# Optimization experiments

Measured on AMD Instinct MI355X. Metric: run time of the kernel, lower is better.

The kernel has to match this reference:

```python
import jax, jax.numpy as jnp
import numpy as np

B, IN, OUT, E, CTX, DEMO = 32768, 512, 128, 16, 256, 16
HID = IN // 2
GATE_IN = CTX + IN + DEMO  # 784


def setup_inputs() -> dict:
    key = jax.random.key(0)
    ks = jax.random.split(key, 9)
    inp = {
        'x': jax.random.normal(ks[0], (B, IN), dtype=jnp.float32),
        'u': jax.random.normal(ks[1], (B, CTX), dtype=jnp.float32),
        'd': jax.random.normal(ks[2], (B, DEMO), dtype=jnp.float32),
        # gate Linear(GATE_IN -> E)
        'gate_W': jax.random.normal(ks[3], (E, GATE_IN), dtype=jnp.float32) * 0.02,
        'gate_b': jnp.zeros((E,), dtype=jnp.float32),
        # per-expert MLP: Linear(IN->HID), ReLU, Linear(HID->OUT); stacked over experts
        'W1': jax.random.normal(ks[4], (E, HID, IN), dtype=jnp.float32) * 0.02,
        'b1': jnp.zeros((E, HID), dtype=jnp.float32),
        'W2': jax.random.normal(ks[5], (E, OUT, HID), dtype=jnp.float32) * 0.02,
        'b2': jnp.zeros((E, OUT), dtype=jnp.float32),
    }
    return inp


def reference(x, u, d, gate_W, gate_b, W1, b1, W2, b2):
    # gate input = cat([u, x, d], dim=1)  -> [B, GATE_IN]
    g_in = jnp.concatenate([u, x, d], axis=1)
    gate_logits = g_in @ gate_W.T + gate_b            # [B, E]
    weights = jax.nn.softmax(gate_logits, axis=1)     # [B, E]
    # all-expert MLP as batched GEMMs
    h = jax.nn.relu(jnp.einsum('bi,ehi->beh', x, W1) + b1[None])   # [B, E, HID]
    expert_outputs = jnp.einsum('beh,eoh->beo', h, W2) + b2[None]  # [B, E, OUT]
    # mixture_mode == 'logits': weighted sum over experts
    out = jnp.einsum('be,beo->bo', weights, expert_outputs)        # [B, OUT]
    return out
```

## Files before the change

kernel.cpp:

```cpp
#include <hip/hip_runtime.h>

#define B_    32768
#define IN_   512
#define HID_  256
#define OUT_  128
#define E_    16
#define CTX_  256
#define DEMO_ 16
#define GIN_  784

typedef __attribute__((ext_vector_type(8))) short short8;
typedef __attribute__((ext_vector_type(4))) float floatx4;

__device__ __forceinline__ short f2bf(float x){
  unsigned u = __builtin_bit_cast(unsigned, x);
  u += 0x7FFFu + ((u >> 16) & 1u);
  return (short)(u >> 16);
}

__device__ __forceinline__ short8 pack8(float4 a, float4 b){
  short8 r;
  r[0]=f2bf(a.x); r[1]=f2bf(a.y); r[2]=f2bf(a.z); r[3]=f2bf(a.w);
  r[4]=f2bf(b.x); r[5]=f2bf(b.y); r[6]=f2bf(b.z); r[7]=f2bf(b.w);
  return r;
}

__device__ __forceinline__ void load_lds16(const short* g, short* l){
  __builtin_amdgcn_global_load_lds((const __attribute__((address_space(1))) void*)g,
                                   (__attribute__((address_space(3))) void*)l,
                                   16, 0, 0);
}

#define VMCNT8()  asm volatile("s_waitcnt vmcnt(8)"  ::: "memory")
#define VMCNT0()  asm volatile("s_waitcnt vmcnt(0)"  ::: "memory")
#define BAR() do{ asm volatile("" ::: "memory"); __builtin_amdgcn_s_barrier(); \
                  asm volatile("" ::: "memory"); }while(0)
#define LGKM0() do{ asm volatile("s_waitcnt lgkmcnt(0)" ::: "memory"); \
                    __builtin_amdgcn_sched_barrier(0); }while(0)

__device__ __forceinline__ void stage128x64(short* lds, const short* g, int gpitch, int tid){
  const int wvv = tid >> 6, ln = tid & 63;
  const int cb = ln & 7, rsub = ln >> 3;
  #pragma unroll
  for (int i = 0; i < 4; ++i){
    const int r0  = (wvv*4 + i)*8;
    const int row = r0 + rsub;
    const short* gp = g + (size_t)row*gpitch + ((cb ^ rsub) << 3);
    load_lds16(gp, lds + r0*64);
  }
}

__global__ void convert_kernel(const float* __restrict__ x, const float* __restrict__ w1,
                               const float* __restrict__ w2, short* __restrict__ xb,
                               short* __restrict__ w1b, short* __restrict__ w2b){
  const int N1 = B_*IN_, N2 = E_*HID_*IN_, N3 = E_*OUT_*HID_;
  const int total4 = (N1 + N2 + N3) >> 2;
  for (int i = blockIdx.x*blockDim.x + threadIdx.x; i < total4; i += gridDim.x*blockDim.x){
    int e4 = i << 2;
    const float* src; short* dst; int off;
    if (e4 < N1)            { src = x;  dst = xb;  off = e4; }
    else if (e4 < N1 + N2)  { src = w1; dst = w1b; off = e4 - N1; }
    else                    { src = w2; dst = w2b; off = e4 - (N1 + N2); }
    float4 v = *(const float4*)(src + off);
    *(short4*)(dst + off) = make_short4(f2bf(v.x), f2bf(v.y), f2bf(v.z), f2bf(v.w));
  }
}

__global__ __launch_bounds__(256)
void gate_kernel(const float* __restrict__ u, const short* __restrict__ xb,
                 const float* __restrict__ d, const float* __restrict__ gW,
                 const float* __restrict__ gb, float* __restrict__ wout){
  const int tid  = threadIdx.x;
  const int wave = tid >> 6, lane = tid & 63;
  const int l15  = lane & 15, quad = lane >> 4;
  const int row0 = blockIdx.x*64 + wave*16;
  const int rA   = row0 + l15;
  const int kq   = quad*8;

  floatx4 acc  = {0.f,0.f,0.f,0.f};
  floatx4 acc2 = {0.f,0.f,0.f,0.f};

  #pragma unroll
  for (int t = 0; t < 8; ++t){
    const float4 a0 = *(const float4*)&u[(size_t)rA*CTX_ + t*32 + kq];
    const float4 a1 = *(const float4*)&u[(size_t)rA*CTX_ + t*32 + kq + 4];
    const float4 b0 = *(const float4*)&gW[(size_t)l15*GIN_ + t*32 + kq];
    const float4 b1 = *(const float4*)&gW[(size_t)l15*GIN_ + t*32 + kq + 4];
    acc = __builtin_amdgcn_mfma_f32_16x16x32_bf16(pack8(a0,a1), pack8(b0,b1), acc, 0,0,0);
  }
  #pragma unroll
  for (int t = 0; t < 16; ++t){
    const short8 af = *(const short8*)&xb[(size_t)rA*IN_ + t*32 + kq];
    const float4 b0 = *(const float4*)&gW[(size_t)l15*GIN_ + 256 + t*32 + kq];
    const float4 b1 = *(const float4*)&gW[(size_t)l15*GIN_ + 256 + t*32 + kq + 4];
    acc2 = __builtin_amdgcn_mfma_f32_16x16x32_bf16(af, pack8(b0,b1), acc2, 0,0,0);
  }
  {
    short8 af = {0,0,0,0,0,0,0,0}, bf = {0,0,0,0,0,0,0,0};
    if (quad < 2){
      const float4 a0 = *(const float4*)&d[(size_t)rA*DEMO_ + kq];
      const float4 a1 = *(const float4*)&d[(size_t)rA*DEMO_ + kq + 4];
      const float4 b0 = *(const float4*)&gW[(size_t)l15*GIN_ + 768 + kq];
      const float4 b1 = *(const float4*)&gW[(size_t)l15*GIN_ + 768 + kq + 4];
      af = pack8(a0,a1); bf = pack8(b0,b1);
    }
    acc = __builtin_amdgcn_mfma_f32_16x16x32_bf16(af, bf, acc, 0,0,0);
  }

  const float bias = gb[l15];
  #pragma unroll
  for (int r = 0; r < 4; ++r){
    float v = acc[r] + acc2[r] + bias;
    float m = v;
    #pragma unroll
    for (int s = 1; s <= 8; s <<= 1) m = fmaxf(m, __shfl_xor(m, s));
    const float p = __expf(v - m);
    float ssum = p;
    #pragma unroll
    for (int s = 1; s <= 8; s <<= 1) ssum += __shfl_xor(ssum, s);
    wout[(size_t)(row0 + quad*4 + r)*E_ + l15] = p / ssum;
  }
}

__global__ __launch_bounds__(256, 2)
void moe_kernel(const short* __restrict__ xb, const short* __restrict__ w1b,
                const short* __restrict__ w2b, const float* __restrict__ gatew,
                const float* __restrict__ b1g, const float* __restrict__ b2g,
                float* __restrict__ out){
  __shared__ alignas(16) char smem[65536];
  short* s_h  = (short*)smem;
  short* s_w2 = (short*)(smem + 32768);

  const int tid  = threadIdx.x;
  const int wv   = tid >> 6;
  const int lane = tid & 63;
  const int l15  = lane & 15;
  const int hi2  = lane >> 4;
  const int r7   = l15 & 7;
  const int h_off  = (wv >> 1) * 64;
  const int mb_off = (wv & 1) * 64;
  const int m_off  = (wv >> 1) * 64;
  const int o_off  = (wv & 1) * 64;
  const int blk_m0 = blockIdx.x * 128;
  const int eg = blockIdx.y;

  floatx4 oacc[4][4];
  #pragma unroll
  for (int a = 0; a < 4; ++a)
    #pragma unroll
    for (int b = 0; b < 4; ++b) oacc[a][b] = floatx4{0.f,0.f,0.f,0.f};

  if (eg == 0){
    #pragma unroll 1
    for (int e = 0; e < E_; ++e){
      float b2v[4];
      #pragma unroll
      for (int nt = 0; nt < 4; ++nt) b2v[nt] = b2g[e*OUT_ + o_off + nt*16 + l15];
      #pragma unroll
      for (int mt = 0; mt < 4; ++mt){
        #pragma unroll
        for (int r = 0; r < 4; ++r){
          const float wgt = gatew[(size_t)(blk_m0 + m_off + mt*16 + hi2*4 + r)*E_ + e];
          #pragma unroll
          for (int nt = 0; nt < 4; ++nt) oacc[mt][nt][r] += wgt * b2v[nt];
        }
      }
    }
  }

  const short* xbase = xb + (size_t)blk_m0*IN_;

  #pragma unroll 1
  for (int ei = 0; ei < 4; ++ei){
    const int e = eg*4 + ei;
    #pragma unroll 1
    for (int half = 0; half < 2; ++half){
      const short* w1base = w1b + (size_t)(e*HID_ + half*128) * IN_;
      const short* w2base = w2b + (size_t)e*OUT_*HID_ + half*128;

      floatx4 g1[4][4];
      #pragma unroll
      for (int a = 0; a < 4; ++a)
        #pragma unroll
        for (int b = 0; b < 4; ++b) g1[a][b] = floatx4{0.f,0.f,0.f,0.f};

      stage128x64((short*)(smem +      0), xbase,  IN_, tid);
      stage128x64((short*)(smem + 16384), w1base, IN_, tid);

      #pragma unroll 1
      for (int kc = 0; kc < 8; ++kc){
        if (kc < 7){
          char* nb = smem + ((kc + 1) & 1)*32768;
          stage128x64((short*)nb,            xbase  + (kc+1)*64, IN_, tid);
          stage128x64((short*)(nb + 16384),  w1base + (kc+1)*64, IN_, tid);
          VMCNT8();
        } else {
          VMCNT0();
        }
        BAR();
        const short* buf = (const short*)(smem + (kc & 1)*32768);
        __builtin_amdgcn_s_setprio(1);
        #pragma unroll
        for (int ks = 0; ks < 2; ++ks){
          const int kb  = ks*4 + hi2;
          const int swz = (kb ^ r7) << 3;
          short8 af[4], bf[4];
          #pragma unroll
          for (int ht = 0; ht < 4; ++ht)
            af[ht] = *(const short8*)&buf[8192 + (h_off + ht*16 + l15)*64 + swz];
          #pragma unroll
          for (int mt = 0; mt < 4; ++mt)
            bf[mt] = *(const short8*)&buf[(mb_off + mt*16 + l15)*64 + swz];
          #pragma unroll
          for (int ht = 0; ht < 4; ++ht)
            #pragma unroll
            for (int mt = 0; mt < 4; ++mt)
              g1[ht][mt] = __builtin_amdgcn_mfma_f32_16x16x32_bf16(af[ht], bf[mt], g1[ht][mt], 0,0,0);
        }
        __builtin_amdgcn_s_setprio(0);
        LGKM0();
        BAR();
      }

      stage128x64(s_w2,        w2base,      HID_, tid);
      stage128x64(s_w2 + 8192, w2base + 64, HID_, tid);

      {
        float4 b1v[4];
        #pragma unroll
        for (int ht = 0; ht < 4; ++ht)
          b1v[ht] = *(const float4*)&b1g[e*HID_ + half*128 + h_off + ht*16 + hi2*4];
        float wgt[4];
        #pragma unroll
        for (int mt = 0; mt < 4; ++mt)
          wgt[mt] = gatew[(size_t)(blk_m0 + mb_off + mt*16 + l15)*E_ + e];
        #pragma unroll
        for (int ht = 0; ht < 4; ++ht){
          const float b1r[4] = {b1v[ht].x, b1v[ht].y, b1v[ht].z, b1v[ht].w};
          const int hb3 = 2*ht + (hi2 >> 1);
          #pragma unroll
          for (int mt = 0; mt < 4; ++mt){
            short4 pk;
            float v0 = fmaxf(g1[ht][mt][0] + b1r[0], 0.f) * wgt[mt];
            float v1 = fmaxf(g1[ht][mt][1] + b1r[1], 0.f) * wgt[mt];
            float v2 = fmaxf(g1[ht][mt][2] + b1r[2], 0.f) * wgt[mt];
            float v3 = fmaxf(g1[ht][mt][3] + b1r[3], 0.f) * wgt[mt];
            pk.x = f2bf(v0); pk.y = f2bf(v1); pk.z = f2bf(v2); pk.w = f2bf(v3);
            *(short4*)&s_h[(size_t)(mb_off + mt*16 + l15)*128 + h_off
                           + ((hb3 ^ r7) << 3) + (hi2 & 1)*4] = pk;
          }
        }
      }
      asm volatile("s_waitcnt vmcnt(0) lgkmcnt(0)" ::: "memory");
      __builtin_amdgcn_sched_barrier(0);
      BAR();

      __builtin_amdgcn_s_setprio(1);
      #pragma unroll
      for (int kc2 = 0; kc2 < 2; ++kc2){
        const short* wb = s_w2 + kc2*8192;
        #pragma unroll
        for (int ks = 0; ks < 2; ++ks){
          const int kb  = ks*4 + hi2;
          const int swz = (kb ^ r7) << 3;
          short8 af[4], bf[4];
          #pragma unroll
          for (int mt = 0; mt < 4; ++mt)
            af[mt] = *(const short8*)&s_h[(size_t)(m_off + mt*16 + l15)*128 + kc2*64 + swz];
          #pragma unroll
          for (int nt = 0; nt < 4; ++nt)
            bf[nt] = *(const short8*)&wb[(o_off + nt*16 + l15)*64 + swz];
          #pragma unroll
          for (int mt = 0; mt < 4; ++mt)
            #pragma unroll
            for (int nt = 0; nt < 4; ++nt)
              oacc[mt][nt] = __builtin_amdgcn_mfma_f32_16x16x32_bf16(af[mt], bf[nt], oacc[mt][nt], 0,0,0);
        }
      }
      __builtin_amdgcn_s_setprio(0);
      LGKM0();
      BAR();
    }
  }

  #pragma unroll
  for (int mt = 0; mt < 4; ++mt)
    #pragma unroll
    for (int nt = 0; nt < 4; ++nt)
      #pragma unroll
      for (int r = 0; r < 4; ++r)
        atomicAdd(&out[(size_t)(blk_m0 + m_off + mt*16 + hi2*4 + r)*OUT_ + o_off + nt*16 + l15],
                  oacc[mt][nt][r]);
}

extern "C" void kernel_launch(void* const* d_in, const int* in_sizes, int n_in,
                              void* d_out, int out_size, void* d_ws, size_t ws_size,
                              hipStream_t stream){
  const float* x  = (const float*)d_in[0];
  const float* u  = (const float*)d_in[1];
  const float* dd = (const float*)d_in[2];
  const float* gW = (const float*)d_in[3];
  const float* gb = (const float*)d_in[4];
  const float* W1 = (const float*)d_in[5];
  const float* b1 = (const float*)d_in[6];
  const float* W2 = (const float*)d_in[7];
  const float* b2 = (const float*)d_in[8];
  float* out = (float*)d_out;

  short* xb  = (short*)d_ws;
  short* w1b = xb  + (size_t)B_*IN_;
  short* w2b = w1b + (size_t)E_*HID_*IN_;
  float* gw  = (float*)(w2b + (size_t)E_*OUT_*HID_);

  hipMemsetAsync(d_out, 0, (size_t)B_*OUT_*sizeof(float), stream);
  hipLaunchKernelGGL(convert_kernel, dim3(4096), dim3(256), 0, stream, x, W1, W2, xb, w1b, w2b);
  hipLaunchKernelGGL(gate_kernel, dim3(B_/64), dim3(256), 0, stream, u, xb, dd, gW, gb, gw);
  hipLaunchKernelGGL(moe_kernel, dim3(B_/128, 4), dim3(256), 0, stream, xb, w1b, w2b, gw, b1, b2, out);
  (void)in_sizes; (void)n_in; (void)out_size; (void)ws_size;
}
```

Measured before the change: 368.4 us.

## Fuse bf16 conversion with gate kernel and prefetch W2 during GEMM1

Merges the conversion kernel and the gate kernel into one launch. Gate blocks now read fp32 x directly instead of waiting for the converted bf16 copy, so conversion and gating run at the same time. In the MoE kernel, the W2 tile stage is issued during the last GEMM1 k-iteration rather than after the loop, overlapping that load with compute. The b2 bias contribution is now spread across expert groups rather than all done by group 0, which balances that work. Costs are an extra fp32 read of x in the gate path and more complex buffer indexing and wait counts.

```diff
diff --git a/kernel.cpp b/kernel.cpp
--- a/kernel.cpp
+++ b/kernel.cpp
@@ -9,6 +9,9 @@
 #define DEMO_ 16
 #define GIN_  784
 
+#define GATEB_ 512
+#define CONVB_ 2048
+
 typedef __attribute__((ext_vector_type(8))) short short8;
 typedef __attribute__((ext_vector_type(4))) float floatx4;
 
@@ -50,26 +53,29 @@
   }
 }
 
-__global__ void convert_kernel(const float* __restrict__ x, const float* __restrict__ w1,
-                               const float* __restrict__ w2, short* __restrict__ xb,
-                               short* __restrict__ w1b, short* __restrict__ w2b){
-  const int N1 = B_*IN_, N2 = E_*HID_*IN_, N3 = E_*OUT_*HID_;
-  const int total4 = (N1 + N2 + N3) >> 2;
-  for (int i = blockIdx.x*blockDim.x + threadIdx.x; i < total4; i += gridDim.x*blockDim.x){
-    int e4 = i << 2;
-    const float* src; short* dst; int off;
-    if (e4 < N1)            { src = x;  dst = xb;  off = e4; }
-    else if (e4 < N1 + N2)  { src = w1; dst = w1b; off = e4 - N1; }
-    else                    { src = w2; dst = w2b; off = e4 - (N1 + N2); }
-    float4 v = *(const float4*)(src + off);
-    *(short4*)(dst + off) = make_short4(f2bf(v.x), f2bf(v.y), f2bf(v.z), f2bf(v.w));
-  }
-}
-
 __global__ __launch_bounds__(256)
-void gate_kernel(const float* __restrict__ u, const short* __restrict__ xb,
-                 const float* __restrict__ d, const float* __restrict__ gW,
-                 const float* __restrict__ gb, float* __restrict__ wout){
+void convgate_kernel(const float* __restrict__ x, const float* __restrict__ u,
+                     const float* __restrict__ d, const float* __restrict__ gW,
+                     const float* __restrict__ gb,
+                     const float* __restrict__ w1, const float* __restrict__ w2,
+                     short* __restrict__ xb, short* __restrict__ w1b,
+                     short* __restrict__ w2b, float* __restrict__ wout){
+  if (blockIdx.x >= GATEB_){
+    const int N1 = B_*IN_, N2 = E_*HID_*IN_, N3 = E_*OUT_*HID_;
+    const int total4 = (N1 + N2 + N3) >> 2;
+    for (int i = (blockIdx.x - GATEB_)*blockDim.x + threadIdx.x; i < total4;
+         i += CONVB_*blockDim.x){
+      int e4 = i << 2;
+      const float* src; short* dst; int off;
+      if (e4 < N1)            { src = x;  dst = xb;  off = e4; }
+      else if (e4 < N1 + N2)  { src = w1; dst = w1b; off = e4 - N1; }
+      else                    { src = w2; dst = w2b; off = e4 - (N1 + N2); }
+      float4 v = *(const float4*)(src + off);
+      *(short4*)(dst + off) = make_short4(f2bf(v.x), f2bf(v.y), f2bf(v.z), f2bf(v.w));
+    }
+    return;
+  }
+
   const int tid  = threadIdx.x;
   const int wave = tid >> 6, lane = tid & 63;
   const int l15  = lane & 15, quad = lane >> 4;
@@ -90,10 +96,11 @@
   }
   #pragma unroll
   for (int t = 0; t < 16; ++t){
-    const short8 af = *(const short8*)&xb[(size_t)rA*IN_ + t*32 + kq];
+    const float4 a0 = *(const float4*)&x[(size_t)rA*IN_ + t*32 + kq];
+    const float4 a1 = *(const float4*)&x[(size_t)rA*IN_ + t*32 + kq + 4];
     const float4 b0 = *(const float4*)&gW[(size_t)l15*GIN_ + 256 + t*32 + kq];
     const float4 b1 = *(const float4*)&gW[(size_t)l15*GIN_ + 256 + t*32 + kq + 4];
-    acc2 = __builtin_amdgcn_mfma_f32_16x16x32_bf16(af, pack8(b0,b1), acc2, 0,0,0);
+    acc2 = __builtin_amdgcn_mfma_f32_16x16x32_bf16(pack8(a0,a1), pack8(b0,b1), acc2, 0,0,0);
   }
   {
     short8 af = {0,0,0,0,0,0,0,0}, bf = {0,0,0,0,0,0,0,0};
@@ -150,20 +157,19 @@
     #pragma unroll
     for (int b = 0; b < 4; ++b) oacc[a][b] = floatx4{0.f,0.f,0.f,0.f};
 
-  if (eg == 0){
-    #pragma unroll 1
-    for (int e = 0; e < E_; ++e){
-      float b2v[4];
+  #pragma unroll 1
+  for (int ei = 0; ei < 4; ++ei){
+    const int e = eg*4 + ei;
+    float b2v[4];
+    #pragma unroll
+    for (int nt = 0; nt < 4; ++nt) b2v[nt] = b2g[e*OUT_ + o_off + nt*16 + l15];
+    #pragma unroll
+    for (int mt = 0; mt < 4; ++mt){
       #pragma unroll
-      for (int nt = 0; nt < 4; ++nt) b2v[nt] = b2g[e*OUT_ + o_off + nt*16 + l15];
-      #pragma unroll
-      for (int mt = 0; mt < 4; ++mt){
-        #pragma unroll
-        for (int r = 0; r < 4; ++r){
-          const float wgt = gatew[(size_t)(blk_m0 + m_off + mt*16 + hi2*4 + r)*E_ + e];
-          #pragma unroll
-          for (int nt = 0; nt < 4; ++nt) oacc[mt][nt][r] += wgt * b2v[nt];
-        }
+      for (int r = 0; r < 4; ++r){
+        const float wgt = gatew[(size_t)(blk_m0 + m_off + mt*16 + hi2*4 + r)*E_ + e];
+        #pragma unroll
+        for (int nt = 0; nt < 4; ++nt) oacc[mt][nt][r] += wgt * b2v[nt];
       }
     }
   }
@@ -184,21 +190,22 @@
         #pragma unroll
         for (int b = 0; b < 4; ++b) g1[a][b] = floatx4{0.f,0.f,0.f,0.f};
 
-      stage128x64((short*)(smem +      0), xbase,  IN_, tid);
-      stage128x64((short*)(smem + 16384), w1base, IN_, tid);
+      stage128x64((short*)(smem + 32768), xbase,  IN_, tid);
+      stage128x64((short*)(smem + 49152), w1base, IN_, tid);
 
       #pragma unroll 1
       for (int kc = 0; kc < 8; ++kc){
         if (kc < 7){
-          char* nb = smem + ((kc + 1) & 1)*32768;
+          char* nb = smem + ((kc + 2) & 1)*32768;
           stage128x64((short*)nb,            xbase  + (kc+1)*64, IN_, tid);
           stage128x64((short*)(nb + 16384),  w1base + (kc+1)*64, IN_, tid);
-          VMCNT8();
         } else {
-          VMCNT0();
+          stage128x64(s_w2,        w2base,      HID_, tid);
+          stage128x64(s_w2 + 8192, w2base + 64, HID_, tid);
         }
+        VMCNT8();
         BAR();
-        const short* buf = (const short*)(smem + (kc & 1)*32768);
+        const short* buf = (const short*)(smem + ((kc + 1) & 1)*32768);
         __builtin_amdgcn_s_setprio(1);
         #pragma unroll
         for (int ks = 0; ks < 2; ++ks){
@@ -221,9 +228,6 @@
         LGKM0();
         BAR();
       }
-
-      stage128x64(s_w2,        w2base,      HID_, tid);
-      stage128x64(s_w2 + 8192, w2base + 64, HID_, tid);
 
       {
         float4 b1v[4];
@@ -251,7 +255,8 @@
           }
         }
       }
-      asm volatile("s_waitcnt vmcnt(0) lgkmcnt(0)" ::: "memory");
+      VMCNT0();
+      asm volatile("s_waitcnt lgkmcnt(0)" ::: "memory");
       __builtin_amdgcn_sched_barrier(0);
       BAR();
 
@@ -313,8 +318,9 @@
   float* gw  = (float*)(w2b + (size_t)E_*OUT_*HID_);
 
   hipMemsetAsync(d_out, 0, (size_t)B_*OUT_*sizeof(float), stream);
-  hipLaunchKernelGGL(convert_kernel, dim3(4096), dim3(256), 0, stream, x, W1, W2, xb, w1b, w2b);
-  hipLaunchKernelGGL(gate_kernel, dim3(B_/64), dim3(256), 0, stream, u, xb, dd, gW, gb, gw);
-  hipLaunchKernelGGL(moe_kernel, dim3(B_/128, 4), dim3(256), 0, stream, xb, w1b, w2b, gw, b1, b2, out);
+  hipLaunchKernelGGL(convgate_kernel, dim3(GATEB_ + CONVB_), dim3(256), 0, stream,
+                     x, u, dd, gW, gb, W1, W2, xb, w1b, w2b, gw);
+  hipLaunchKernelGGL(moe_kernel, dim3(B_/128, 4), dim3(256), 0, stream,
+                     xb, w1b, w2b, gw, b1, b2, out);
   (void)in_sizes; (void)n_in; (void)out_size; (void)ws_size;
 }
```

Result: slower. 382.3 us (+3.8%).

## Halve K-chunk to 32, shrink LDS to 48KB for 3 blocks/CU, pipeline W2 loads

Applied to the files above, without the earlier changes.

The GEMM1 K-loop now stages 128x32 tiles instead of 128x64, which cuts LDS from 64KB to 48KB and raises launch bounds to 3 blocks per CU. The W2 tile staging is moved into the last GEMM1 iteration and split into four 32-wide chunks so the second GEMM overlaps its loads. B fragments are loaded one at a time to lower register pressure. The b2 bias contribution is now split across all expert groups instead of only group 0. The trade-off is more barriers and iterations per tile, and register limits under 3-block occupancy could cause spills.

```diff
diff --git a/kernel.cpp b/kernel.cpp
--- a/kernel.cpp
+++ b/kernel.cpp
@@ -31,22 +31,23 @@
                                    16, 0, 0);
 }
 
-#define VMCNT8()  asm volatile("s_waitcnt vmcnt(8)"  ::: "memory")
+#define VMCNT4()  asm volatile("s_waitcnt vmcnt(4)"  ::: "memory")
+#define VMCNT2()  asm volatile("s_waitcnt vmcnt(2)"  ::: "memory")
 #define VMCNT0()  asm volatile("s_waitcnt vmcnt(0)"  ::: "memory")
 #define BAR() do{ asm volatile("" ::: "memory"); __builtin_amdgcn_s_barrier(); \
                   asm volatile("" ::: "memory"); }while(0)
 #define LGKM0() do{ asm volatile("s_waitcnt lgkmcnt(0)" ::: "memory"); \
                     __builtin_amdgcn_sched_barrier(0); }while(0)
 
-__device__ __forceinline__ void stage128x64(short* lds, const short* g, int gpitch, int tid){
+__device__ __forceinline__ void stage128x32(short* lds, const short* g, int gpitch, int tid){
   const int wvv = tid >> 6, ln = tid & 63;
-  const int cb = ln & 7, rsub = ln >> 3;
-  #pragma unroll
-  for (int i = 0; i < 4; ++i){
-    const int r0  = (wvv*4 + i)*8;
+  const int cb = ln & 3, rsub = ln >> 2;
+  #pragma unroll
+  for (int i = 0; i < 2; ++i){
+    const int r0  = (wvv*2 + i)*16;
     const int row = r0 + rsub;
-    const short* gp = g + (size_t)row*gpitch + ((cb ^ rsub) << 3);
-    load_lds16(gp, lds + r0*64);
+    const short* gp = g + (size_t)row*gpitch + ((cb ^ (row & 3)) << 3);
+    load_lds16(gp, lds + r0*32);
   }
 }
 
@@ -122,12 +123,12 @@
   }
 }
 
-__global__ __launch_bounds__(256, 2)
+__global__ __launch_bounds__(256, 3)
 void moe_kernel(const short* __restrict__ xb, const short* __restrict__ w1b,
                 const short* __restrict__ w2b, const float* __restrict__ gatew,
                 const float* __restrict__ b1g, const float* __restrict__ b2g,
                 float* __restrict__ out){
-  __shared__ alignas(16) char smem[65536];
+  __shared__ alignas(16) char smem[49152];
   short* s_h  = (short*)smem;
   short* s_w2 = (short*)(smem + 32768);
 
@@ -137,6 +138,7 @@
   const int l15  = lane & 15;
   const int hi2  = lane >> 4;
   const int r7   = l15 & 7;
+  const int swb  = (hi2 ^ (l15 & 3)) << 3;
   const int h_off  = (wv >> 1) * 64;
   const int mb_off = (wv & 1) * 64;
   const int m_off  = (wv >> 1) * 64;
@@ -150,20 +152,19 @@
     #pragma unroll
     for (int b = 0; b < 4; ++b) oacc[a][b] = floatx4{0.f,0.f,0.f,0.f};
 
-  if (eg == 0){
-    #pragma unroll 1
-    for (int e = 0; e < E_; ++e){
-      float b2v[4];
+  #pragma unroll 1
+  for (int ei = 0; ei < 4; ++ei){
+    const int e = eg*4 + ei;
+    float b2v[4];
+    #pragma unroll
+    for (int nt = 0; nt < 4; ++nt) b2v[nt] = b2g[e*OUT_ + o_off + nt*16 + l15];
+    #pragma unroll
+    for (int mt = 0; mt < 4; ++mt){
       #pragma unroll
-      for (int nt = 0; nt < 4; ++nt) b2v[nt] = b2g[e*OUT_ + o_off + nt*16 + l15];
-      #pragma unroll
-      for (int mt = 0; mt < 4; ++mt){
-        #pragma unroll
-        for (int r = 0; r < 4; ++r){
-          const float wgt = gatew[(size_t)(blk_m0 + m_off + mt*16 + hi2*4 + r)*E_ + e];
-          #pragma unroll
-          for (int nt = 0; nt < 4; ++nt) oacc[mt][nt][r] += wgt * b2v[nt];
-        }
+      for (int r = 0; r < 4; ++r){
+        const float wgt = gatew[(size_t)(blk_m0 + m_off + mt*16 + hi2*4 + r)*E_ + e];
+        #pragma unroll
+        for (int nt = 0; nt < 4; ++nt) oacc[mt][nt][r] += wgt * b2v[nt];
       }
     }
   }
@@ -184,46 +185,40 @@
         #pragma unroll
         for (int b = 0; b < 4; ++b) g1[a][b] = floatx4{0.f,0.f,0.f,0.f};
 
-      stage128x64((short*)(smem +      0), xbase,  IN_, tid);
-      stage128x64((short*)(smem + 16384), w1base, IN_, tid);
+      stage128x32((short*)smem,        xbase,  IN_, tid);
+      stage128x32((short*)smem + 4096, w1base, IN_, tid);
 
       #pragma unroll 1
-      for (int kc = 0; kc < 8; ++kc){
-        if (kc < 7){
-          char* nb = smem + ((kc + 1) & 1)*32768;
-          stage128x64((short*)nb,            xbase  + (kc+1)*64, IN_, tid);
-          stage128x64((short*)(nb + 16384),  w1base + (kc+1)*64, IN_, tid);
-          VMCNT8();
+      for (int kc = 0; kc < 16; ++kc){
+        if (kc < 15){
+          short* nb = (short*)(smem + ((kc + 1) & 1)*16384);
+          stage128x32(nb,        xbase  + (kc+1)*32, IN_, tid);
+          stage128x32(nb + 4096, w1base + (kc+1)*32, IN_, tid);
         } else {
-          VMCNT0();
+          stage128x32(s_w2,        w2base,      HID_, tid);
+          stage128x32(s_w2 + 4096, w2base + 32, HID_, tid);
         }
+        VMCNT4();
         BAR();
-        const short* buf = (const short*)(smem + (kc & 1)*32768);
+        const short* buf = (const short*)(smem + (kc & 1)*16384);
         __builtin_amdgcn_s_setprio(1);
-        #pragma unroll
-        for (int ks = 0; ks < 2; ++ks){
-          const int kb  = ks*4 + hi2;
-          const int swz = (kb ^ r7) << 3;
-          short8 af[4], bf[4];
+        {
+          short8 af[4];
           #pragma unroll
           for (int ht = 0; ht < 4; ++ht)
-            af[ht] = *(const short8*)&buf[8192 + (h_off + ht*16 + l15)*64 + swz];
-          #pragma unroll
-          for (int mt = 0; mt < 4; ++mt)
-            bf[mt] = *(const short8*)&buf[(mb_off + mt*16 + l15)*64 + swz];
-          #pragma unroll
-          for (int ht = 0; ht < 4; ++ht)
+            af[ht] = *(const short8*)&buf[4096 + (h_off + ht*16 + l15)*32 + swb];
+          #pragma unroll
+          for (int mt = 0; mt < 4; ++mt){
+            const short8 bf = *(const short8*)&buf[(mb_off + mt*16 + l15)*32 + swb];
             #pragma unroll
-            for (int mt = 0; mt < 4; ++mt)
-              g1[ht][mt] = __builtin_amdgcn_mfma_f32_16x16x32_bf16(af[ht], bf[mt], g1[ht][mt], 0,0,0);
+            for (int ht = 0; ht < 4; ++ht)
+              g1[ht][mt] = __builtin_amdgcn_mfma_f32_16x16x32_bf16(af[ht], bf, g1[ht][mt], 0,0,0);
+          }
         }
         __builtin_amdgcn_s_setprio(0);
         LGKM0();
         BAR();
       }
-
-      stage128x64(s_w2,        w2base,      HID_, tid);
-      stage128x64(s_w2 + 8192, w2base + 64, HID_, tid);
 
       {
         float4 b1v[4];
@@ -251,35 +246,40 @@
           }
         }
       }
-      asm volatile("s_waitcnt vmcnt(0) lgkmcnt(0)" ::: "memory");
+      VMCNT0();
+      asm volatile("s_waitcnt lgkmcnt(0)" ::: "memory");
       __builtin_amdgcn_sched_barrier(0);
       BAR();
 
-      __builtin_amdgcn_s_setprio(1);
-      #pragma unroll
-      for (int kc2 = 0; kc2 < 2; ++kc2){
-        const short* wb = s_w2 + kc2*8192;
-        #pragma unroll
-        for (int ks = 0; ks < 2; ++ks){
-          const int kb  = ks*4 + hi2;
-          const int swz = (kb ^ r7) << 3;
-          short8 af[4], bf[4];
+      #pragma unroll 1
+      for (int c = 0; c < 4; ++c){
+        if (c == 1)      stage128x32(s_w2,        w2base + 64, HID_, tid);
+        else if (c == 2){ stage128x32(s_w2 + 4096, w2base + 96, HID_, tid);
+                          VMCNT2();
+                          BAR(); }
+        else if (c == 3){ VMCNT0();
+                          BAR(); }
+        const short* wb = s_w2 + (c & 1)*4096;
+        const int halfsel = (c >> 1)*64;
+        const int swzA = ((((c & 1)*4 + hi2) ^ r7) << 3);
+        __builtin_amdgcn_s_setprio(1);
+        {
+          short8 af[4];
           #pragma unroll
           for (int mt = 0; mt < 4; ++mt)
-            af[mt] = *(const short8*)&s_h[(size_t)(m_off + mt*16 + l15)*128 + kc2*64 + swz];
-          #pragma unroll
-          for (int nt = 0; nt < 4; ++nt)
-            bf[nt] = *(const short8*)&wb[(o_off + nt*16 + l15)*64 + swz];
-          #pragma unroll
-          for (int mt = 0; mt < 4; ++mt)
+            af[mt] = *(const short8*)&s_h[(size_t)(m_off + mt*16 + l15)*128 + halfsel + swzA];
+          #pragma unroll
+          for (int nt = 0; nt < 4; ++nt){
+            const short8 bf = *(const short8*)&wb[(o_off + nt*16 + l15)*32 + swb];
             #pragma unroll
-            for (int nt = 0; nt < 4; ++nt)
-              oacc[mt][nt] = __builtin_amdgcn_mfma_f32_16x16x32_bf16(af[mt], bf[nt], oacc[mt][nt], 0,0,0);
+            for (int mt = 0; mt < 4; ++mt)
+              oacc[mt][nt] = __builtin_amdgcn_mfma_f32_16x16x32_bf16(af[mt], bf, oacc[mt][nt], 0,0,0);
+          }
         }
+        __builtin_amdgcn_s_setprio(0);
+        LGKM0();
+        BAR();
       }
-      __builtin_amdgcn_s_setprio(0);
-      LGKM0();
-      BAR();
     }
   }
 
```

Result: slower. 571.0 us (+55.0%).
